# Kernel tuning notes

Measured on AMD Instinct MI355X. Metric: run time of the kernel, lower is better.

## Reference

```python
import jax, jax.numpy as jnp
import numpy as np
import math

B, S, D, H = 4, 1024, 1024, 16
DK = D // H


def setup_inputs() -> dict:
    key = jax.random.key(0)
    ks = jax.random.split(key, 14)
    inp = {
        "query": jax.random.normal(ks[0], (B, S, D), dtype=jnp.float32),
        "key": jax.random.normal(ks[1], (B, S, D), dtype=jnp.float32),
        "value": jax.random.normal(ks[2], (B, S, D), dtype=jnp.float32),
        "attention_bias": jax.random.normal(ks[3], (B, S, S, H), dtype=jnp.float32),
        "mask": jax.random.randint(ks[4], (B, S), 0, 2).astype(bool),
    }
    scale = 0.02
    inp["Wq"] = jax.random.normal(ks[5], (D, D), dtype=jnp.float32) * scale
    inp["bq"] = jnp.zeros((D,), dtype=jnp.float32)
    inp["Wk"] = jax.random.normal(ks[6], (D, D), dtype=jnp.float32) * scale
    inp["bk"] = jnp.zeros((D,), dtype=jnp.float32)
    inp["Wv"] = jax.random.normal(ks[7], (D, D), dtype=jnp.float32) * scale
    inp["bv"] = jnp.zeros((D,), dtype=jnp.float32)
    inp["Wo"] = jax.random.normal(ks[8], (D, D), dtype=jnp.float32) * scale
    inp["bo"] = jnp.zeros((D,), dtype=jnp.float32)
    return inp


def reference(query, key, value, attention_bias, mask, Wq, bq, Wk, bk, Wv, bv, Wo, bo):
    # projections (torch Linear: x @ W.T + b), split heads -> [B,H,S,DK]
    def proj(x, W, b):
        y = x @ W.T + b
        return y.reshape(B, S, H, DK).transpose(0, 2, 1, 3)

    q = proj(query, Wq, bq)
    k = proj(key, Wk, bk)
    v = proj(value, Wv, bv)

    bias = attention_bias.transpose(0, 3, 1, 2)  # [B,H,S,S]
    scores = (jnp.einsum("bhqd,bhkd->bhqk", q, k) + bias) / math.sqrt(DK)

    # pairwise mask: outer product of per-token mask, broadcast over heads
    pm = (mask[:, None, :, None] & mask[:, None, None, :])  # [B,1,S,S]
    scores = jnp.where(pm, scores, jnp.float32(-1e9))

    p_attn = jax.nn.softmax(scores, axis=-1)  # dropout is identity in eval
    x = jnp.einsum("bhqk,bhkd->bhqd", p_attn, v)
    x = x.transpose(0, 2, 1, 3).reshape(B, S, D)
    return x @ Wo.T + bo
```

## Files before the change

kernel.cpp:

```cpp
#include <hip/hip_runtime.h>
#include <hip/hip_bf16.h>
#include <math.h>

#define B_ 4
#define S_ 1024
#define D_ 1024
#define H_ 16
#define DK_ 64

typedef short bf16x8 __attribute__((ext_vector_type(8)));
typedef float f32x4 __attribute__((ext_vector_type(4)));

#define MFMA(a, b, c) __builtin_amdgcn_mfma_f32_16x16x32_bf16(a, b, c, 0, 0, 0)

#define GLDS(gp, lp)                                                        \
    __builtin_amdgcn_global_load_lds(                                       \
        (const __attribute__((address_space(1))) void*)(const void*)(gp),   \
        (__attribute__((address_space(3))) void*)(void*)(lp), 16, 0, 0)

static __device__ __forceinline__ unsigned short f2bf(float f) {
    __hip_bfloat16 h = __float2bfloat16(f);
    return *reinterpret_cast<unsigned short*>(&h);
}

__global__ __launch_bounds__(256) void cvt_bf16(
    const float* __restrict__ in, unsigned short* __restrict__ out, int n4)
{
    int i = blockIdx.x * 256 + threadIdx.x;
    if (i >= n4) return;
    float4 v = ((const float4*)in)[i];
    ushort4 o;
    o.x = f2bf(v.x); o.y = f2bf(v.y); o.z = f2bf(v.z); o.w = f2bf(v.w);
    ((ushort4*)out)[i] = o;
}

__global__ __launch_bounds__(256, 2) void gemm_mfma(
    const unsigned short* __restrict__ X, const unsigned short* __restrict__ W,
    const float* __restrict__ bvec, void* __restrict__ Yv, int mode)
{
    __shared__ unsigned short As[128 * 32];
    __shared__ unsigned short Bs[64 * 32];

    const int t = threadIdx.x;
    const int w = t >> 6, l = t & 63;
    const int lane16 = l & 15, quad = l >> 4;
    const int m0 = blockIdx.y * 128, n0 = blockIdx.x * 64;
    const int wr = w >> 1, wc = w & 1;

    const int arow = w * 16 + (l >> 2);
    const unsigned short* agp = X + (size_t)(m0 + arow) * 1024 + (l & 3) * 8;
    unsigned short* alp = As + w * 512 + l * 8;
    const unsigned short* bgp = W + (size_t)(n0 + arow) * 1024 + (l & 3) * 8;
    unsigned short* blp = Bs + w * 512 + l * 8;

    f32x4 zero = {0.f, 0.f, 0.f, 0.f};
    f32x4 acc[4][2];
    #pragma unroll
    for (int i = 0; i < 4; ++i)
        #pragma unroll
        for (int j = 0; j < 2; ++j) acc[i][j] = zero;

    for (int kt = 0; kt < 1024; kt += 32) {
        GLDS(agp + kt, alp);
        GLDS(agp + kt + 64 * 1024, alp + 64 * 32);
        GLDS(bgp + kt, blp);
        __syncthreads();

        bf16x8 af[4], bf[2];
        #pragma unroll
        for (int i = 0; i < 4; ++i)
            af[i] = *(const bf16x8*)(As + (wr * 64 + i * 16 + lane16) * 32 + quad * 8);
        #pragma unroll
        for (int j = 0; j < 2; ++j)
            bf[j] = *(const bf16x8*)(Bs + (wc * 32 + j * 16 + lane16) * 32 + quad * 8);

        #pragma unroll
        for (int i = 0; i < 4; ++i)
            #pragma unroll
            for (int j = 0; j < 2; ++j)
                acc[i][j] = MFMA(af[i], bf[j], acc[i][j]);
        __syncthreads();
    }

    float bv[2];
    #pragma unroll
    for (int j = 0; j < 2; ++j) bv[j] = bvec[n0 + wc * 32 + j * 16 + lane16];

    #pragma unroll
    for (int i = 0; i < 4; ++i) {
        #pragma unroll
        for (int j = 0; j < 2; ++j) {
            int n = n0 + wc * 32 + j * 16 + lane16;
            #pragma unroll
            for (int r = 0; r < 4; ++r) {
                size_t m = m0 + wr * 64 + i * 16 + quad * 4 + r;
                float val = acc[i][j][r] + bv[j];
                if (mode == 0) {
                    ((unsigned short*)Yv)[m * 1024 + n] = f2bf(val);
                } else if (mode == 1) {
                    int b = (int)(m >> 10), s = (int)(m & 1023);
                    int h = n >> 6, dk = n & 63;
                    ((unsigned short*)Yv)[(((size_t)(b * 16 + h) * 64 + dk) << 10) + s] = f2bf(val);
                } else {
                    ((float*)Yv)[m * 1024 + n] = val;
                }
            }
        }
    }
}

__global__ __launch_bounds__(256, 2) void attn_mfma(
    const unsigned short* __restrict__ Qp, const unsigned short* __restrict__ Kp,
    const unsigned short* __restrict__ VpT, const float* __restrict__ bias,
    const int* __restrict__ mask, unsigned short* __restrict__ Xp)
{
    __shared__ unsigned short Ks[64 * 64];
    __shared__ unsigned short Vs[64 * 64];
    __shared__ unsigned short Ps[4][16 * 72];

    const int t = threadIdx.x;
    const int w = t >> 6, l = t & 63;
    const int lane16 = l & 15, quad = l >> 4;

    const int bid = blockIdx.x;
    const int r8 = bid & 7, v_ = bid >> 3;
    const int h = v_ & 15;
    const int g = ((v_ >> 4) << 3) + r8;
    const int qt = g & 15, b = g >> 4;
    const int q0 = qt * 64;
    const int qrow0 = q0 + w * 16;

    bf16x8 qf[2];
    #pragma unroll
    for (int c = 0; c < 2; ++c)
        qf[c] = *(const bf16x8*)(Qp + (size_t)(b * 1024 + qrow0 + lane16) * 1024
                                 + h * 64 + c * 32 + quad * 8);

    int mrow[4];
    size_t brow[4];
    #pragma unroll
    for (int r = 0; r < 4; ++r) {
        int qg = qrow0 + quad * 4 + r;
        mrow[r] = mask[b * 1024 + qg];
        brow[r] = ((size_t)(b * 1024 + qg) * 1024) * 16 + h;
    }

    const int krow = w * 8 + (l >> 3);
    const int kgran = (l & 7) ^ ((l >> 3) & 7);
    const unsigned short* kg = Kp + ((size_t)(b * 1024 + krow) * 16 + h) * 64 + kgran * 8;
    unsigned short* klp = Ks + w * 512 + l * 8;
    const unsigned short* vg = VpT + ((size_t)(b * 16 + h) * 64 + krow) * 1024 + kgran * 8;
    unsigned short* vlp = Vs + w * 512 + l * 8;

    f32x4 zero = {0.f, 0.f, 0.f, 0.f};
    f32x4 o[4];
    #pragma unroll
    for (int j = 0; j < 4; ++j) o[j] = zero;
    float m_i[4] = {-1e30f, -1e30f, -1e30f, -1e30f};
    float l_i[4] = {0.f, 0.f, 0.f, 0.f};

    for (int k0 = 0; k0 < 1024; k0 += 64) {
        GLDS(kg + (size_t)k0 * 1024, klp);
        GLDS(kg + (size_t)(k0 + 32) * 1024, klp + 32 * 64);
        GLDS(vg + k0, vlp);
        GLDS(vg + k0 + 32 * 1024, vlp + 32 * 64);
        __syncthreads();

        float bvv[4][4];
        int mk[4];
        #pragma unroll
        for (int j = 0; j < 4; ++j) {
            int keyg = k0 + j * 16 + lane16;
            mk[j] = mask[b * 1024 + keyg];
            #pragma unroll
            for (int r = 0; r < 4; ++r)
                bvv[j][r] = bias[brow[r] + (size_t)keyg * 16];
        }

        f32x4 s[4];
        #pragma unroll
        for (int j = 0; j < 4; ++j) {
            s[j] = zero;
            #pragma unroll
            for (int c = 0; c < 2; ++c) {
                bf16x8 kf = *(const bf16x8*)(Ks + (j * 16 + lane16) * 64
                                             + (((c * 4 + quad) ^ (lane16 & 7)) * 8));
                s[j] = MFMA(qf[c], kf, s[j]);
            }
        }

        float sc[4][4];
        #pragma unroll
        for (int j = 0; j < 4; ++j)
            #pragma unroll
            for (int r = 0; r < 4; ++r)
                sc[j][r] = (mrow[r] && mk[j]) ? (s[j][r] + bvv[j][r]) * 0.125f : -1e9f;

        float p[4][4];
        #pragma unroll
        for (int r = 0; r < 4; ++r) {
            float mx = fmaxf(fmaxf(sc[0][r], sc[1][r]), fmaxf(sc[2][r], sc[3][r]));
            #pragma unroll
            for (int d = 1; d < 16; d <<= 1) mx = fmaxf(mx, __shfl_xor(mx, d, 64));
            float mnew = fmaxf(m_i[r], mx);
            float alpha = __expf(m_i[r] - mnew);
            m_i[r] = mnew;
            float sum = 0.f;
            #pragma unroll
            for (int j = 0; j < 4; ++j) {
                p[j][r] = __expf(sc[j][r] - mnew);
                sum += p[j][r];
            }
            #pragma unroll
            for (int d = 1; d < 16; d <<= 1) sum += __shfl_xor(sum, d, 64);
            l_i[r] = l_i[r] * alpha + sum;
            #pragma unroll
            for (int jd = 0; jd < 4; ++jd) o[jd][r] *= alpha;
        }

        #pragma unroll
        for (int j = 0; j < 4; ++j)
            #pragma unroll
            for (int r = 0; r < 4; ++r)
                Ps[w][(quad * 4 + r) * 72 + j * 16 + lane16] = f2bf(p[j][r]);
        asm volatile("" ::: "memory");

        bf16x8 pf[2];
        #pragma unroll
        for (int c = 0; c < 2; ++c)
            pf[c] = *(const bf16x8*)(&Ps[w][lane16 * 72 + c * 32 + quad * 8]);

        #pragma unroll
        for (int jd = 0; jd < 4; ++jd)
            #pragma unroll
            for (int c = 0; c < 2; ++c) {
                bf16x8 vf = *(const bf16x8*)(Vs + (jd * 16 + lane16) * 64
                                             + (((c * 4 + quad) ^ (lane16 & 7)) * 8));
                o[jd] = MFMA(pf[c], vf, o[jd]);
            }
        __syncthreads();
    }

    float inv[4];
    #pragma unroll
    for (int r = 0; r < 4; ++r) inv[r] = 1.0f / l_i[r];

    #pragma unroll
    for (int jd = 0; jd < 4; ++jd)
        #pragma unroll
        for (int r = 0; r < 4; ++r)
            Xp[(size_t)(b * 1024 + qrow0 + quad * 4 + r) * 1024
               + h * 64 + jd * 16 + lane16] = f2bf(o[jd][r] * inv[r]);
}

extern "C" void kernel_launch(void* const* d_in, const int* in_sizes, int n_in,
                              void* d_out, int out_size, void* d_ws, size_t ws_size,
                              hipStream_t stream)
{
    const float* query = (const float*)d_in[0];
    const float* key   = (const float*)d_in[1];
    const float* value = (const float*)d_in[2];
    const float* abias = (const float*)d_in[3];
    const int*   mask  = (const int*)d_in[4];
    const float* Wq = (const float*)d_in[5];
    const float* bq = (const float*)d_in[6];
    const float* Wk = (const float*)d_in[7];
    const float* bk = (const float*)d_in[8];
    const float* Wv = (const float*)d_in[9];
    const float* bv = (const float*)d_in[10];
    const float* Wo = (const float*)d_in[11];
    const float* bo = (const float*)d_in[12];
    float* out = (float*)d_out;

    const size_t T = (size_t)B_ * S_ * D_;
    const size_t WSZ = (size_t)D_ * D_;
    unsigned short* p = (unsigned short*)d_ws;
    unsigned short* qb  = p;  p += T;
    unsigned short* kb  = p;  p += T;
    unsigned short* vb  = p;  p += T;
    unsigned short* wqb = p;  p += WSZ;
    unsigned short* wkb = p;  p += WSZ;
    unsigned short* wvb = p;  p += WSZ;
    unsigned short* wob = p;  p += WSZ;
    unsigned short* Qpj = p;  p += T;
    unsigned short* Kpj = p;  p += T;
    unsigned short* VpT = p;  p += T;
    unsigned short* Xpj = p;  p += T;

    cvt_bf16<<<dim3((int)(T / 4 / 256)), 256, 0, stream>>>(query, qb, (int)(T / 4));
    cvt_bf16<<<dim3((int)(T / 4 / 256)), 256, 0, stream>>>(key,   kb, (int)(T / 4));
    cvt_bf16<<<dim3((int)(T / 4 / 256)), 256, 0, stream>>>(value, vb, (int)(T / 4));
    cvt_bf16<<<dim3((int)(WSZ / 4 / 256)), 256, 0, stream>>>(Wq, wqb, (int)(WSZ / 4));
    cvt_bf16<<<dim3((int)(WSZ / 4 / 256)), 256, 0, stream>>>(Wk, wkb, (int)(WSZ / 4));
    cvt_bf16<<<dim3((int)(WSZ / 4 / 256)), 256, 0, stream>>>(Wv, wvb, (int)(WSZ / 4));
    cvt_bf16<<<dim3((int)(WSZ / 4 / 256)), 256, 0, stream>>>(Wo, wob, (int)(WSZ / 4));

    dim3 gg(16, 32);
    gemm_mfma<<<gg, 256, 0, stream>>>(qb, wqb, bq, Qpj, 0);
    gemm_mfma<<<gg, 256, 0, stream>>>(kb, wkb, bk, Kpj, 0);
    gemm_mfma<<<gg, 256, 0, stream>>>(vb, wvb, bv, VpT, 1);

    attn_mfma<<<dim3(1024), 256, 0, stream>>>(Qpj, Kpj, VpT, abias, mask, Xpj);

    gemm_mfma<<<gg, 256, 0, stream>>>(Xpj, wob, bo, out, 2);
}
```

Measured before the change: 637.5 us.

## Prepack masked bias to bf16 fragments, batch QKV GEMMs with 128x128 tiles

Adds a pre-pass that converts the fp32 attention bias and pairwise mask into a bf16, pre-scaled tensor laid out in MFMA fragment order, so the attention kernel loads two contiguous vectors per tile instead of strided fp32 gathers plus mask checks. The scale and row mask are folded into the Q projection epilogue. The QKV projections run as one z-batched GEMM with 128x128 tiles, and the conversion kernels are merged. This trades an extra full pass over the bias and lower bias precision for cheaper attention inner loops and fewer launches.

```diff
diff --git a/kernel.cpp b/kernel.cpp
--- a/kernel.cpp
+++ b/kernel.cpp
@@ -22,87 +22,195 @@
     __hip_bfloat16 h = __float2bfloat16(f);
     return *reinterpret_cast<unsigned short*>(&h);
 }
-
-__global__ __launch_bounds__(256) void cvt_bf16(
-    const float* __restrict__ in, unsigned short* __restrict__ out, int n4)
-{
-    int i = blockIdx.x * 256 + threadIdx.x;
-    if (i >= n4) return;
+static __device__ __forceinline__ float bf2f(unsigned short u) {
+    unsigned int x = ((unsigned int)u) << 16;
+    union { unsigned int i; float f; } c; c.i = x; return c.f;
+}
+
+__global__ __launch_bounds__(256) void cvt3(
+    const float* __restrict__ a, const float* __restrict__ b, const float* __restrict__ c,
+    unsigned short* __restrict__ oa, unsigned short* __restrict__ ob, unsigned short* __restrict__ oc)
+{
+    int bx = blockIdx.x;
+    int which = bx >> 12;
+    const float* in = which == 0 ? a : which == 1 ? b : c;
+    unsigned short* out = which == 0 ? oa : which == 1 ? ob : oc;
+    int i = (bx & 4095) * 256 + threadIdx.x;
     float4 v = ((const float4*)in)[i];
     ushort4 o;
     o.x = f2bf(v.x); o.y = f2bf(v.y); o.z = f2bf(v.z); o.w = f2bf(v.w);
     ((ushort4*)out)[i] = o;
 }
 
-__global__ __launch_bounds__(256, 2) void gemm_mfma(
-    const unsigned short* __restrict__ X, const unsigned short* __restrict__ W,
-    const float* __restrict__ bvec, void* __restrict__ Yv, int mode)
+__global__ __launch_bounds__(256) void cvt4(
+    const float* __restrict__ a, const float* __restrict__ b,
+    const float* __restrict__ c, const float* __restrict__ d,
+    unsigned short* __restrict__ oa, unsigned short* __restrict__ ob,
+    unsigned short* __restrict__ oc, unsigned short* __restrict__ od)
+{
+    int bx = blockIdx.x;
+    int which = bx >> 10;
+    const float* in = which == 0 ? a : which == 1 ? b : which == 2 ? c : d;
+    unsigned short* out = which == 0 ? oa : which == 1 ? ob : which == 2 ? oc : od;
+    int i = (bx & 1023) * 256 + threadIdx.x;
+    float4 v = ((const float4*)in)[i];
+    ushort4 o;
+    o.x = f2bf(v.x); o.y = f2bf(v.y); o.z = f2bf(v.z); o.w = f2bf(v.w);
+    ((ushort4*)out)[i] = o;
+}
+
+__global__ __launch_bounds__(256) void prep_bias(
+    const float* __restrict__ bias, const int* __restrict__ mask,
+    unsigned short* __restrict__ biasP)
+{
+    const int t = threadIdx.x;
+    const int h = t & 15, u = t >> 4;
+    const int x = blockIdx.x;
+    const int kt = x & 15, q16 = (x >> 4) & 63, b = x >> 10;
+
+    const unsigned short NEG = f2bf(-28672.f);
+
+    int mk[4];
+    #pragma unroll
+    for (int j = 0; j < 4; ++j) mk[j] = mask[b * 1024 + kt * 64 + j * 16 + u];
+
+    const float* bb = bias + (((size_t)(b * 1024 + q16 * 16) * 1024) + kt * 64) * 16 + h;
+    unsigned short* ob = biasP + ((((size_t)(b * 16 + h) * 64 + q16) * 16 + kt) * 64) * 16;
+
+    #pragma unroll
+    for (int quad = 0; quad < 4; ++quad) {
+        bf16x8 v0, v1;
+        #pragma unroll
+        for (int r = 0; r < 4; ++r) {
+            int q = quad * 4 + r;
+            int mq = mask[b * 1024 + q16 * 16 + q];
+            #pragma unroll
+            for (int j = 0; j < 4; ++j) {
+                float v = bb[((size_t)q * 1024 + j * 16 + u) * 16];
+                unsigned short pv = (mq && mk[j]) ? f2bf(v * 0.125f) : NEG;
+                if (j < 2) v0[j * 4 + r] = (short)pv;
+                else       v1[(j - 2) * 4 + r] = (short)pv;
+            }
+        }
+        unsigned short* dst = ob + (size_t)(quad * 16 + u) * 16;
+        *(bf16x8*)(dst) = v0;
+        *(bf16x8*)(dst + 8) = v1;
+    }
+}
+
+__global__ __launch_bounds__(256, 2) void gemm128(
+    const unsigned short* __restrict__ X0, const unsigned short* __restrict__ X1,
+    const unsigned short* __restrict__ X2,
+    const unsigned short* __restrict__ W0, const unsigned short* __restrict__ W1,
+    const unsigned short* __restrict__ W2,
+    const float* __restrict__ bv0, const float* __restrict__ bv1,
+    const float* __restrict__ bv2,
+    void* __restrict__ Y0, void* __restrict__ Y1, void* __restrict__ Y2,
+    const int* __restrict__ mask, int mode_ovr)
 {
     __shared__ unsigned short As[128 * 32];
-    __shared__ unsigned short Bs[64 * 32];
+    __shared__ unsigned short Bs[128 * 32];
+
+    const int z = blockIdx.z;
+    const unsigned short* X = z == 0 ? X0 : z == 1 ? X1 : X2;
+    const unsigned short* W = z == 0 ? W0 : z == 1 ? W1 : W2;
+    const float* bvec = z == 0 ? bv0 : z == 1 ? bv1 : bv2;
+    void* Yv = z == 0 ? Y0 : z == 1 ? Y1 : Y2;
+    const int mode = mode_ovr >= 0 ? mode_ovr : z;
 
     const int t = threadIdx.x;
     const int w = t >> 6, l = t & 63;
     const int lane16 = l & 15, quad = l >> 4;
-    const int m0 = blockIdx.y * 128, n0 = blockIdx.x * 64;
+    const int m0 = blockIdx.y * 128, n0 = blockIdx.x * 128;
     const int wr = w >> 1, wc = w & 1;
 
-    const int arow = w * 16 + (l >> 2);
-    const unsigned short* agp = X + (size_t)(m0 + arow) * 1024 + (l & 3) * 8;
+    const int srow = w * 16 + (l >> 2);
+    const unsigned short* agp = X + (size_t)(m0 + srow) * 1024 + (l & 3) * 8;
+    const unsigned short* bgp = W + (size_t)(n0 + srow) * 1024 + (l & 3) * 8;
     unsigned short* alp = As + w * 512 + l * 8;
-    const unsigned short* bgp = W + (size_t)(n0 + arow) * 1024 + (l & 3) * 8;
     unsigned short* blp = Bs + w * 512 + l * 8;
 
     f32x4 zero = {0.f, 0.f, 0.f, 0.f};
-    f32x4 acc[4][2];
+    f32x4 acc[4][4];
     #pragma unroll
     for (int i = 0; i < 4; ++i)
         #pragma unroll
-        for (int j = 0; j < 2; ++j) acc[i][j] = zero;
+        for (int j = 0; j < 4; ++j) acc[i][j] = zero;
 
     for (int kt = 0; kt < 1024; kt += 32) {
         GLDS(agp + kt, alp);
-        GLDS(agp + kt + 64 * 1024, alp + 64 * 32);
+        GLDS(agp + kt + 64 * 1024, alp + 2048);
         GLDS(bgp + kt, blp);
+        GLDS(bgp + kt + 64 * 1024, blp + 2048);
         __syncthreads();
 
-        bf16x8 af[4], bf[2];
+        bf16x8 af[4], bfv[4];
         #pragma unroll
         for (int i = 0; i < 4; ++i)
             af[i] = *(const bf16x8*)(As + (wr * 64 + i * 16 + lane16) * 32 + quad * 8);
         #pragma unroll
-        for (int j = 0; j < 2; ++j)
-            bf[j] = *(const bf16x8*)(Bs + (wc * 32 + j * 16 + lane16) * 32 + quad * 8);
+        for (int j = 0; j < 4; ++j)
+            bfv[j] = *(const bf16x8*)(Bs + (wc * 64 + j * 16 + lane16) * 32 + quad * 8);
 
         #pragma unroll
         for (int i = 0; i < 4; ++i)
             #pragma unroll
-            for (int j = 0; j < 2; ++j)
-                acc[i][j] = MFMA(af[i], bf[j], acc[i][j]);
+            for (int j = 0; j < 4; ++j)
+                acc[i][j] = MFMA(af[i], bfv[j], acc[i][j]);
         __syncthreads();
     }
 
-    float bv[2];
-    #pragma unroll
-    for (int j = 0; j < 2; ++j) bv[j] = bvec[n0 + wc * 32 + j * 16 + lane16];
-
-    #pragma unroll
-    for (int i = 0; i < 4; ++i) {
-        #pragma unroll
-        for (int j = 0; j < 2; ++j) {
-            int n = n0 + wc * 32 + j * 16 + lane16;
-            #pragma unroll
-            for (int r = 0; r < 4; ++r) {
-                size_t m = m0 + wr * 64 + i * 16 + quad * 4 + r;
-                float val = acc[i][j][r] + bv[j];
-                if (mode == 0) {
-                    ((unsigned short*)Yv)[m * 1024 + n] = f2bf(val);
-                } else if (mode == 1) {
-                    int b = (int)(m >> 10), s = (int)(m & 1023);
-                    int h = n >> 6, dk = n & 63;
-                    ((unsigned short*)Yv)[(((size_t)(b * 16 + h) * 64 + dk) << 10) + s] = f2bf(val);
-                } else {
-                    ((float*)Yv)[m * 1024 + n] = val;
+    float bvl[4];
+    #pragma unroll
+    for (int j = 0; j < 4; ++j) bvl[j] = bvec[n0 + wc * 64 + j * 16 + lane16];
+
+    if (mode == 2) {
+        const int bb = m0 >> 10;
+        const int sb = (m0 & 1023) + wr * 64;
+        #pragma unroll
+        for (int i = 0; i < 4; ++i) {
+            #pragma unroll
+            for (int j = 0; j < 4; ++j) {
+                int n = n0 + wc * 64 + j * 16 + lane16;
+                ushort4 pk;
+                pk.x = f2bf(acc[i][j][0] + bvl[j]);
+                pk.y = f2bf(acc[i][j][1] + bvl[j]);
+                pk.z = f2bf(acc[i][j][2] + bvl[j]);
+                pk.w = f2bf(acc[i][j][3] + bvl[j]);
+                int s = sb + i * 16 + quad * 4;
+                *(ushort4*)((unsigned short*)Yv + ((size_t)(bb * 1024 + n)) * 1024 + s) = pk;
+            }
+        }
+    } else if (mode == 3) {
+        float* Y = (float*)Yv;
+        #pragma unroll
+        for (int i = 0; i < 4; ++i)
+            #pragma unroll
+            for (int j = 0; j < 4; ++j) {
+                int n = n0 + wc * 64 + j * 16 + lane16;
+                #pragma unroll
+                for (int r = 0; r < 4; ++r) {
+                    size_t m = m0 + wr * 64 + i * 16 + quad * 4 + r;
+                    Y[m * 1024 + n] = acc[i][j][r] + bvl[j];
+                }
+            }
+    } else {
+        unsigned short* Y = (unsigned short*)Yv;
+        #pragma unroll
+        for (int i = 0; i < 4; ++i) {
+            int mrow[4];
+            #pragma unroll
+            for (int r = 0; r < 4; ++r)
+                mrow[r] = (mode == 0) ? mask[m0 + wr * 64 + i * 16 + quad * 4 + r] : 1;
+            #pragma unroll
+            for (int j = 0; j < 4; ++j) {
+                int n = n0 + wc * 64 + j * 16 + lane16;
+                #pragma unroll
+                for (int r = 0; r < 4; ++r) {
+                    size_t m = m0 + wr * 64 + i * 16 + quad * 4 + r;
+                    float val = acc[i][j][r] + bvl[j];
+                    if (mode == 0) val = mrow[r] ? val * 0.125f : 0.f;
+                    Y[m * 1024 + n] = f2bf(val);
                 }
             }
         }
@@ -111,8 +219,8 @@
 
 __global__ __launch_bounds__(256, 2) void attn_mfma(
     const unsigned short* __restrict__ Qp, const unsigned short* __restrict__ Kp,
-    const unsigned short* __restrict__ VpT, const float* __restrict__ bias,
-    const int* __restrict__ mask, unsigned short* __restrict__ Xp)
+    const unsigned short* __restrict__ VpT, const unsigned short* __restrict__ biasP,
+    unsigned short* __restrict__ Xp)
 {
     __shared__ unsigned short Ks[64 * 64];
     __shared__ unsigned short Vs[64 * 64];
@@ -123,12 +231,11 @@
     const int lane16 = l & 15, quad = l >> 4;
 
     const int bid = blockIdx.x;
-    const int r8 = bid & 7, v_ = bid >> 3;
-    const int h = v_ & 15;
-    const int g = ((v_ >> 4) << 3) + r8;
-    const int qt = g & 15, b = g >> 4;
+    const int bh = bid & 63, qt = bid >> 6;
+    const int h = bh & 15, b = bh >> 4;
     const int q0 = qt * 64;
     const int qrow0 = q0 + w * 16;
+    const int q16 = qt * 4 + w;
 
     bf16x8 qf[2];
     #pragma unroll
@@ -136,18 +243,12 @@
         qf[c] = *(const bf16x8*)(Qp + (size_t)(b * 1024 + qrow0 + lane16) * 1024
                                  + h * 64 + c * 32 + quad * 8);
 
-    int mrow[4];
-    size_t brow[4];
-    #pragma unroll
-    for (int r = 0; r < 4; ++r) {
-        int qg = qrow0 + quad * 4 + r;
-        mrow[r] = mask[b * 1024 + qg];
-        brow[r] = ((size_t)(b * 1024 + qg) * 1024) * 16 + h;
-    }
+    const unsigned short* bp = biasP
+        + ((((size_t)(b * 16 + h) * 64 + q16) * 16) * 64 + l) * 16;
 
     const int krow = w * 8 + (l >> 3);
     const int kgran = (l & 7) ^ ((l >> 3) & 7);
-    const unsigned short* kg = Kp + ((size_t)(b * 1024 + krow) * 16 + h) * 64 + kgran * 8;
+    const unsigned short* kg = Kp + (size_t)(b * 1024 + krow) * 1024 + h * 64 + kgran * 8;
     unsigned short* klp = Ks + w * 512 + l * 8;
     const unsigned short* vg = VpT + ((size_t)(b * 16 + h) * 64 + krow) * 1024 + kgran * 8;
     unsigned short* vlp = Vs + w * 512 + l * 8;
@@ -159,23 +260,16 @@
     float m_i[4] = {-1e30f, -1e30f, -1e30f, -1e30f};
     float l_i[4] = {0.f, 0.f, 0.f, 0.f};
 
-    for (int k0 = 0; k0 < 1024; k0 += 64) {
+    for (int kt16 = 0; kt16 < 16; ++kt16) {
+        const int k0 = kt16 * 64;
         GLDS(kg + (size_t)k0 * 1024, klp);
         GLDS(kg + (size_t)(k0 + 32) * 1024, klp + 32 * 64);
         GLDS(vg + k0, vlp);
         GLDS(vg + k0 + 32 * 1024, vlp + 32 * 64);
+
+        bf16x8 bfr0 = *(const bf16x8*)(bp + (size_t)kt16 * 1024);
+        bf16x8 bfr1 = *(const bf16x8*)(bp + (size_t)kt16 * 1024 + 8);
         __syncthreads();
-
-        float bvv[4][4];
-        int mk[4];
-        #pragma unroll
-        for (int j = 0; j < 4; ++j) {
-            int keyg = k0 + j * 16 + lane16;
-            mk[j] = mask[b * 1024 + keyg];
-            #pragma unroll
-            for (int r = 0; r < 4; ++r)
-                bvv[j][r] = bias[brow[r] + (size_t)keyg * 16];
-        }
 
         f32x4 s[4];
         #pragma unroll
@@ -191,10 +285,10 @@
 
         float sc[4][4];
         #pragma unroll
-        for (int j = 0; j < 4; ++j)
-            #pragma unroll
-            for (int r = 0; r < 4; ++r)
-                sc[j][r] = (mrow[r] && mk[j]) ? (s[j][r] + bvv[j][r]) * 0.125f : -1e9f;
+        for (int e = 0; e < 8; ++e) {
+            sc[e >> 2][e & 3]       = s[e >> 2][e & 3]       + bf2f((unsigned short)bfr0[e]);
+            sc[2 + (e >> 2)][e & 3] = s[2 + (e >> 2)][e & 3] + bf2f((unsigned short)bfr1[e]);
+        }
 
         float p[4][4];
         #pragma unroll
@@ -274,7 +368,9 @@
 
     const size_t T = (size_t)B_ * S_ * D_;
     const size_t WSZ = (size_t)D_ * D_;
+    const size_t BPSZ = (size_t)B_ * H_ * S_ * S_;
     unsigned short* p = (unsigned short*)d_ws;
+    unsigned short* biasP = p;  p += BPSZ;
     unsigned short* qb  = p;  p += T;
     unsigned short* kb  = p;  p += T;
     unsigned short* vb  = p;  p += T;
@@ -287,20 +383,17 @@
     unsigned short* VpT = p;  p += T;
     unsigned short* Xpj = p;  p += T;
 
-    cvt_bf16<<<dim3((int)(T / 4 / 256)), 256, 0, stream>>>(query, qb, (int)(T / 4));
-    cvt_bf16<<<dim3((int)(T / 4 / 256)), 256, 0, stream>>>(key,   kb, (int)(T / 4));
-    cvt_bf16<<<dim3((int)(T / 4 / 256)), 256, 0, stream>>>(value, vb, (int)(T / 4));
-    cvt_bf16<<<dim3((int)(WSZ / 4 / 256)), 256, 0, stream>>>(Wq, wqb, (int)(WSZ / 4));
-    cvt_bf16<<<dim3((int)(WSZ / 4 / 256)), 256, 0, stream>>>(Wk, wkb, (int)(WSZ / 4));
-    cvt_bf16<<<dim3((int)(WSZ / 4 / 256)), 256, 0, stream>>>(Wv, wvb, (int)(WSZ / 4));
-    cvt_bf16<<<dim3((int)(WSZ / 4 / 256)), 256, 0, stream>>>(Wo, wob, (int)(WSZ / 4));
-
-    dim3 gg(16, 32);
-    gemm_mfma<<<gg, 256, 0, stream>>>(qb, wqb, bq, Qpj, 0);
-    gemm_mfma<<<gg, 256, 0, stream>>>(kb, wkb, bk, Kpj, 0);
-    gemm_mfma<<<gg, 256, 0, stream>>>(vb, wvb, bv, VpT, 1);
-
-    attn_mfma<<<dim3(1024), 256, 0, stream>>>(Qpj, Kpj, VpT, abias, mask, Xpj);
-
-    gemm_mfma<<<gg, 256, 0, stream>>>(Xpj, wob, bo, out, 2);
-}
+    cvt3<<<dim3(3 * 4096), 256, 0, stream>>>(query, key, value, qb, kb, vb);
+    cvt4<<<dim3(4 * 1024), 256, 0, stream>>>(Wq, Wk, Wv, Wo, wqb, wkb, wvb, wob);
+    prep_bias<<<dim3(4096), 256, 0, stream>>>(abias, mask, biasP);
+
+    gemm128<<<dim3(8, 32, 3), 256, 0, stream>>>(
+        qb, kb, vb, wqb, wkb, wvb, bq, bk, bv,
+        (void*)Qpj, (void*)Kpj, (void*)VpT, mask, -1);
+
+    attn_mfma<<<dim3(1024), 256, 0, stream>>>(Qpj, Kpj, VpT, biasP, Xpj);
+
+    gemm128<<<dim3(8, 32, 1), 256, 0, stream>>>(
+        Xpj, Xpj, Xpj, wob, wob, wob, bo, bo, bo,
+        (void*)out, (void*)out, (void*)out, mask, 3);
+}
```

After: 582.9 us. 1.09x faster.
